# Kernel tuning notes

Measured on AMD Instinct MI355X. Metric: run time of the kernel, lower is better.

## Reference

```python
import jax, jax.numpy as jnp
import numpy as np

DIM = 512
H = 8
D = DIM // H  # head_dim = 64
B, N = 2, 2048


def setup_inputs() -> dict:
    key = jax.random.key(0)
    ks = jax.random.split(key, 12)
    s = 1.0 / np.sqrt(DIM)
    inp = {
        "x": jax.random.normal(ks[0], (B, N, DIM), jnp.float32),
        "geo_bias": jax.random.normal(ks[1], (B, H, N, N), jnp.float32),
        "Wq": jax.random.normal(ks[2], (DIM, DIM), jnp.float32) * s,
        "bq": jnp.zeros((DIM,), jnp.float32),
        "Wk": jax.random.normal(ks[3], (DIM, DIM), jnp.float32) * s,
        "bk": jnp.zeros((DIM,), jnp.float32),
        "Wv": jax.random.normal(ks[4], (DIM, DIM), jnp.float32) * s,
        "bv": jnp.zeros((DIM,), jnp.float32),
        "Wo": jax.random.normal(ks[5], (DIM, DIM), jnp.float32) * s,
        "bo": jnp.zeros((DIM,), jnp.float32),
    }
    return inp


def reference(x, geo_bias, Wq, bq, Wk, bk, Wv, bv, Wo, bo):
    # x: (B, N, dim); geo_bias: (B, H, N, N)
    scale = D ** -0.5
    q = (x @ Wq.T + bq).reshape(B, N, H, D)
    k = (x @ Wk.T + bk).reshape(B, N, H, D)
    v = (x @ Wv.T + bv).reshape(B, N, H, D)
    # scores: (B, H, N, N)
    attn = jnp.einsum("bihd,bjhd->bhij", q, k) * scale + geo_bias
    attn = jax.nn.softmax(attn, axis=-1)
    out = jnp.einsum("bhij,bjhd->bihd", attn, v).reshape(B, N, DIM)
    return out @ Wo.T + bo
```

## Files before the change

kernel.cpp:

```cpp
#include <hip/hip_runtime.h>
#include <math.h>

#define SCALE 0.125f

typedef __bf16 bf16;
typedef __bf16 bf16x8 __attribute__((ext_vector_type(8)));
typedef float f32x4 __attribute__((ext_vector_type(4)));

#define WS_XB   0u
#define WS_WB   4194304u
#define WS_Q    6291456u
#define WS_K    10485760u
#define WS_VT   14680064u
#define WS_AT   18874368u

__global__ __launch_bounds__(256) void convert_kernel(
    const float* __restrict__ x, const float* __restrict__ wq,
    const float* __restrict__ wk, const float* __restrict__ wv,
    const float* __restrict__ wo, bf16* __restrict__ xb, bf16* __restrict__ wb) {
  int i = blockIdx.x * 256 + threadIdx.x;
  const float4* src; bf16* dst; int off;
  if (i < 524288) { src = (const float4*)x; dst = xb; off = i; }
  else {
    int j = i - 524288;
    int wsel = j >> 16; off = j & 65535;
    const float* wl = wsel == 0 ? wq : wsel == 1 ? wk : wsel == 2 ? wv : wo;
    src = (const float4*)wl; dst = wb + (wsel << 18);
  }
  float4 v = src[off];
  union { bf16 h[4]; uint2 u; } tmp;
  tmp.h[0] = (bf16)v.x; tmp.h[1] = (bf16)v.y;
  tmp.h[2] = (bf16)v.z; tmp.h[3] = (bf16)v.w;
  ((uint2*)dst)[off] = tmp.u;
}

__global__ __launch_bounds__(256) void qkv_gemm(
    const bf16* __restrict__ xb, const bf16* __restrict__ wb,
    const float* __restrict__ bq, const float* __restrict__ bk,
    const float* __restrict__ bv, bf16* __restrict__ qws,
    bf16* __restrict__ kws, bf16* __restrict__ vtws) {
  __shared__ bf16 Al[128 * 40];
  __shared__ bf16 Bl[128 * 40];
  int t = threadIdx.x;
  int m0 = (blockIdx.x & 31) << 7;
  int n0 = (blockIdx.x >> 5) << 7;
  int lane = t & 63, w = t >> 6;
  int quad = lane >> 4, col = lane & 15;
  int mblk = (w >> 1) * 64, nblk = (w & 1) * 64;
  f32x4 acc[4][4] = {};
  for (int k0 = 0; k0 < 512; k0 += 32) {
    __syncthreads();
    for (int pass = 0; pass < 2; ++pass) {
      int c = t + (pass << 8);
      int row = c >> 2, part = c & 3;
      *(uint4*)&Al[row * 40 + part * 8] =
          *(const uint4*)&xb[(m0 + row) * 512 + k0 + part * 8];
      *(uint4*)&Bl[row * 40 + part * 8] =
          *(const uint4*)&wb[(n0 + row) * 512 + k0 + part * 8];
    }
    __syncthreads();
    bf16x8 af[4], bfv[4];
    for (int i = 0; i < 4; i++)
      af[i] = *(const bf16x8*)&Al[(mblk + i * 16 + col) * 40 + quad * 8];
    for (int i = 0; i < 4; i++)
      bfv[i] = *(const bf16x8*)&Bl[(nblk + i * 16 + col) * 40 + quad * 8];
    for (int mi = 0; mi < 4; mi++)
      for (int ni = 0; ni < 4; ni++)
        acc[mi][ni] = __builtin_amdgcn_mfma_f32_16x16x32_bf16(
            af[mi], bfv[ni], acc[mi][ni], 0, 0, 0);
  }
  for (int mi = 0; mi < 4; mi++)
    for (int ni = 0; ni < 4; ni++) {
      int n = n0 + nblk + ni * 16 + col;
      int wid = n >> 9, feat = n & 511;
      float bias = wid == 0 ? bq[feat] : wid == 1 ? bk[feat] : bv[feat];
      int h = feat >> 6, d = feat & 63;
      int mbase = m0 + mblk + mi * 16 + quad * 4;
      int bidx = mbase >> 11, seq0 = mbase & 2047;
      if (wid == 2) {
        union { bf16 h4[4]; ushort4 u4; } pk;
        for (int r = 0; r < 4; r++) pk.h4[r] = (bf16)(acc[mi][ni][r] + bias);
        *(ushort4*)&vtws[(size_t)((((bidx << 3) + h) << 6) + d) * 2048 + seq0] = pk.u4;
      } else {
        bf16* dst = wid == 0 ? qws : kws;
        for (int r = 0; r < 4; r++)
          dst[(size_t)((((bidx << 3) + h) << 11) + seq0 + r) * 64 + d] =
              (bf16)(acc[mi][ni][r] + bias);
      }
    }
}

__global__ __launch_bounds__(256, 2) void attn_kernel(
    const bf16* __restrict__ qws, const bf16* __restrict__ kws,
    const bf16* __restrict__ vtws, const float* __restrict__ gbias,
    bf16* __restrict__ attn) {
  __shared__ bf16 Kl[2][64 * 72];
  __shared__ bf16 Vl[2][64 * 72];
  __shared__ bf16 Pl[64 * 72];
  int t = threadIdx.x, lane = t & 63, w = t >> 6;
  int quad = lane >> 4, col = lane & 15;
  int bh = blockIdx.x >> 5, qt = blockIdx.x & 31;
  int q0 = qt << 6;
  const bf16* qbase = qws + (size_t)bh * 2048 * 64;
  const bf16* kbase = kws + (size_t)bh * 2048 * 64;
  const bf16* vbase = vtws + (size_t)bh * 64 * 2048;
  const float* bb = gbias + ((size_t)bh * 2048 + q0) * 2048;

  int srow = t >> 2;
  int scol = (t & 3) << 4;

  bf16x8 aq[2];
  for (int ks = 0; ks < 2; ++ks)
    aq[ks] = *(const bf16x8*)&qbase[(q0 + w * 16 + col) * 64 + ks * 32 + quad * 8];

  f32x4 o[4] = {};
  float mrow[4], lrow[4];
  for (int r = 0; r < 4; r++) { mrow[r] = -INFINITY; lrow[r] = 0.f; }

  float bc[2][16];
  for (int r = 0; r < 4; r++)
    for (int nt = 0; nt < 4; nt++) {
      const float* brow = bb + (size_t)(w * 16 + quad * 4 + r) * 2048;
      bc[0][r * 4 + nt] = brow[nt * 16 + col];
      bc[1][r * 4 + nt] = brow[64 + nt * 16 + col];
    }

  {
    *(uint4*)&Kl[0][srow * 72 + scol]     = *(const uint4*)&kbase[srow * 64 + scol];
    *(uint4*)&Kl[0][srow * 72 + scol + 8] = *(const uint4*)&kbase[srow * 64 + scol + 8];
    *(uint4*)&Vl[0][srow * 72 + scol]     = *(const uint4*)&vbase[srow * 2048 + scol];
    *(uint4*)&Vl[0][srow * 72 + scol + 8] = *(const uint4*)&vbase[srow * 2048 + scol + 8];
  }
  __syncthreads();

  for (int kt = 0; kt < 32; kt += 2) {
#pragma unroll
    for (int u = 0; u < 2; ++u) {
      const int cur = u;
      int kt_ = kt + u;
      int snxt = (kt_ + 1) << 6;

      uint4 kra = *(const uint4*)&kbase[(snxt + srow) * 64 + scol];
      uint4 krb = *(const uint4*)&kbase[(snxt + srow) * 64 + scol + 8];
      uint4 vra = *(const uint4*)&vbase[srow * 2048 + snxt + scol];
      uint4 vrb = *(const uint4*)&vbase[srow * 2048 + snxt + scol + 8];

      f32x4 s[4];
#pragma unroll
      for (int nt = 0; nt < 4; ++nt) {
        f32x4 a = {};
#pragma unroll
        for (int ks = 0; ks < 2; ++ks) {
          bf16x8 bk_ = *(const bf16x8*)&Kl[cur][(nt * 16 + col) * 72 + ks * 32 + quad * 8];
          a = __builtin_amdgcn_mfma_f32_16x16x32_bf16(aq[ks], bk_, a, 0, 0, 0);
        }
        s[nt] = a;
      }

      float p[4][4];
#pragma unroll
      for (int r = 0; r < 4; r++) {
        float sv[4];
        float mx = -INFINITY;
#pragma unroll
        for (int nt = 0; nt < 4; nt++) {
          sv[nt] = s[nt][r] * SCALE + bc[cur][r * 4 + nt];
          mx = fmaxf(mx, sv[nt]);
        }
#pragma unroll
        for (int d = 1; d < 16; d <<= 1) mx = fmaxf(mx, __shfl_xor(mx, d));
        float mnew = fmaxf(mrow[r], mx);
        float alpha = __expf(mrow[r] - mnew);
        float sum = 0.f;
#pragma unroll
        for (int nt = 0; nt < 4; nt++) {
          float e = __expf(sv[nt] - mnew);
          p[nt][r] = e; sum += e;
        }
#pragma unroll
        for (int d = 1; d < 16; d <<= 1) sum += __shfl_xor(sum, d);
        lrow[r] = lrow[r] * alpha + sum;
        mrow[r] = mnew;
#pragma unroll
        for (int dt = 0; dt < 4; ++dt) o[dt][r] *= alpha;
      }

      if (kt_ < 30) {
        int sb = (kt_ + 2) << 6;
#pragma unroll
        for (int r = 0; r < 4; r++) {
          const float* brow = bb + (size_t)(w * 16 + quad * 4 + r) * 2048 + sb;
#pragma unroll
          for (int nt = 0; nt < 4; nt++)
            bc[cur][r * 4 + nt] = brow[nt * 16 + col];
        }
      }

#pragma unroll
      for (int nt = 0; nt < 4; nt++)
#pragma unroll
        for (int r = 0; r < 4; r++)
          Pl[(w * 16 + quad * 4 + r) * 72 + nt * 16 + col] = (bf16)p[nt][r];

#pragma unroll
      for (int ks = 0; ks < 2; ++ks) {
        bf16x8 ap = *(const bf16x8*)&Pl[(w * 16 + col) * 72 + ks * 32 + quad * 8];
#pragma unroll
        for (int dt = 0; dt < 4; ++dt) {
          bf16x8 bv_ = *(const bf16x8*)&Vl[cur][(dt * 16 + col) * 72 + ks * 32 + quad * 8];
          o[dt] = __builtin_amdgcn_mfma_f32_16x16x32_bf16(ap, bv_, o[dt], 0, 0, 0);
        }
      }

      int nb = 1 - cur;
      *(uint4*)&Kl[nb][srow * 72 + scol]     = kra;
      *(uint4*)&Kl[nb][srow * 72 + scol + 8] = krb;
      *(uint4*)&Vl[nb][srow * 72 + scol]     = vra;
      *(uint4*)&Vl[nb][srow * 72 + scol + 8] = vrb;
      __syncthreads();
    }
  }

  bf16* obase = attn + (size_t)(bh >> 3) * 2048 * 512 + (bh & 7) * 64;
  for (int r = 0; r < 4; r++) {
    float inv = 1.f / lrow[r];
    int gq = q0 + w * 16 + quad * 4 + r;
    for (int dt = 0; dt < 4; ++dt)
      obase[(size_t)gq * 512 + dt * 16 + col] = (bf16)(o[dt][r] * inv);
  }
}

__global__ __launch_bounds__(256) void out_gemm(
    const bf16* __restrict__ ab, const bf16* __restrict__ wob,
    const float* __restrict__ bo, float* __restrict__ out) {
  __shared__ bf16 Al[128 * 40];
  __shared__ bf16 Bl[128 * 40];
  int t = threadIdx.x;
  int m0 = (blockIdx.x & 31) << 7;
  int n0 = (blockIdx.x >> 5) << 7;
  int lane = t & 63, w = t >> 6;
  int quad = lane >> 4, col = lane & 15;
  int mblk = (w >> 1) * 64, nblk = (w & 1) * 64;
  f32x4 acc[4][4] = {};
  for (int k0 = 0; k0 < 512; k0 += 32) {
    __syncthreads();
    for (int pass = 0; pass < 2; ++pass) {
      int c = t + (pass << 8);
      int row = c >> 2, part = c & 3;
      *(uint4*)&Al[row * 40 + part * 8] =
          *(const uint4*)&ab[(m0 + row) * 512 + k0 + part * 8];
      *(uint4*)&Bl[row * 40 + part * 8] =
          *(const uint4*)&wob[(n0 + row) * 512 + k0 + part * 8];
    }
    __syncthreads();
    bf16x8 af[4], bfv[4];
    for (int i = 0; i < 4; i++)
      af[i] = *(const bf16x8*)&Al[(mblk + i * 16 + col) * 40 + quad * 8];
    for (int i = 0; i < 4; i++)
      bfv[i] = *(const bf16x8*)&Bl[(nblk + i * 16 + col) * 40 + quad * 8];
    for (int mi = 0; mi < 4; mi++)
      for (int ni = 0; ni < 4; ni++)
        acc[mi][ni] = __builtin_amdgcn_mfma_f32_16x16x32_bf16(
            af[mi], bfv[ni], acc[mi][ni], 0, 0, 0);
  }
  for (int mi = 0; mi < 4; mi++)
    for (int ni = 0; ni < 4; ni++)
      for (int r = 0; r < 4; r++) {
        int m = m0 + mblk + mi * 16 + quad * 4 + r;
        int n = n0 + nblk + ni * 16 + col;
        out[(size_t)m * 512 + n] = acc[mi][ni][r] + bo[n];
      }
}

extern "C" void kernel_launch(void* const* d_in, const int* in_sizes, int n_in,
                              void* d_out, int out_size, void* d_ws, size_t ws_size,
                              hipStream_t stream) {
  const float* x  = (const float*)d_in[0];
  const float* gb = (const float*)d_in[1];
  const float* Wq = (const float*)d_in[2];
  const float* bq = (const float*)d_in[3];
  const float* Wk = (const float*)d_in[4];
  const float* bk = (const float*)d_in[5];
  const float* Wv = (const float*)d_in[6];
  const float* bv = (const float*)d_in[7];
  const float* Wo = (const float*)d_in[8];
  const float* bo = (const float*)d_in[9];
  float* out = (float*)d_out;
  char* ws = (char*)d_ws;
  bf16* xb   = (bf16*)(ws + WS_XB);
  bf16* wb   = (bf16*)(ws + WS_WB);
  bf16* qws  = (bf16*)(ws + WS_Q);
  bf16* kws  = (bf16*)(ws + WS_K);
  bf16* vtws = (bf16*)(ws + WS_VT);
  bf16* at   = (bf16*)(ws + WS_AT);

  hipLaunchKernelGGL(convert_kernel, dim3(3072), dim3(256), 0, stream,
                     x, Wq, Wk, Wv, Wo, xb, wb);
  hipLaunchKernelGGL(qkv_gemm, dim3(384), dim3(256), 0, stream,
                     xb, wb, bq, bk, bv, qws, kws, vtws);
  hipLaunchKernelGGL(attn_kernel, dim3(512), dim3(256), 0, stream,
                     qws, kws, vtws, gb, at);
  hipLaunchKernelGGL(out_gemm, dim3(128), dim3(256), 0, stream,
                     at, wb + 3 * 262144, bo, out);
}
```

Measured before the change: 443.4 us.

## Double-buffer GEMM tiles, stage geo bias through LDS, skip redundant softmax rescales

Both GEMMs switch to 128x64 tiles with register-prefetched, double-buffered LDS loads and twice as many blocks, so global loads overlap MFMA work and more CUs are busy. The attention kernel now loads the fp32 geo_bias tile with coalesced float4 reads into a swizzled LDS buffer, replacing strided per-lane scalar loads. It also skips the online-softmax rescale when no row max increases, and raises wave priority around the MFMA sections. The extra 32KB of LDS per block may reduce attention occupancy.

```diff
diff --git a/kernel.cpp b/kernel.cpp
--- a/kernel.cpp
+++ b/kernel.cpp
@@ -39,38 +39,50 @@
     const float* __restrict__ bq, const float* __restrict__ bk,
     const float* __restrict__ bv, bf16* __restrict__ qws,
     bf16* __restrict__ kws, bf16* __restrict__ vtws) {
-  __shared__ bf16 Al[128 * 40];
-  __shared__ bf16 Bl[128 * 40];
+  __shared__ bf16 Al[2][128 * 40];
+  __shared__ bf16 Bl[2][64 * 40];
   int t = threadIdx.x;
   int m0 = (blockIdx.x & 31) << 7;
-  int n0 = (blockIdx.x >> 5) << 7;
+  int n0 = (blockIdx.x >> 5) << 6;
   int lane = t & 63, w = t >> 6;
   int quad = lane >> 4, col = lane & 15;
-  int mblk = (w >> 1) * 64, nblk = (w & 1) * 64;
-  f32x4 acc[4][4] = {};
-  for (int k0 = 0; k0 < 512; k0 += 32) {
+  int mblk = (w >> 1) * 64, nblk = (w & 1) * 32;
+  int arow = t >> 1, apart = (t & 1) << 1;
+  int brow = t >> 2, bpart = t & 3;
+  const bf16* ag = &xb[(m0 + arow) * 512 + apart * 8];
+  const bf16* bg = &wb[(n0 + brow) * 512 + bpart * 8];
+  f32x4 acc[4][2] = {};
+  uint4 ra0 = *(const uint4*)ag;
+  uint4 ra1 = *(const uint4*)(ag + 8);
+  uint4 rb  = *(const uint4*)bg;
+  for (int it = 0; it < 16; ++it) {
+    int cur = it & 1;
+    *(uint4*)&Al[cur][arow * 40 + apart * 8]     = ra0;
+    *(uint4*)&Al[cur][arow * 40 + apart * 8 + 8] = ra1;
+    *(uint4*)&Bl[cur][brow * 40 + bpart * 8]     = rb;
+    if (it < 15) {
+      int k0 = (it + 1) << 5;
+      ra0 = *(const uint4*)(ag + k0);
+      ra1 = *(const uint4*)(ag + k0 + 8);
+      rb  = *(const uint4*)(bg + k0);
+    }
     __syncthreads();
-    for (int pass = 0; pass < 2; ++pass) {
-      int c = t + (pass << 8);
-      int row = c >> 2, part = c & 3;
-      *(uint4*)&Al[row * 40 + part * 8] =
-          *(const uint4*)&xb[(m0 + row) * 512 + k0 + part * 8];
-      *(uint4*)&Bl[row * 40 + part * 8] =
-          *(const uint4*)&wb[(n0 + row) * 512 + k0 + part * 8];
-    }
-    __syncthreads();
-    bf16x8 af[4], bfv[4];
+    bf16x8 af[4], bfv[2];
+#pragma unroll
     for (int i = 0; i < 4; i++)
-      af[i] = *(const bf16x8*)&Al[(mblk + i * 16 + col) * 40 + quad * 8];
-    for (int i = 0; i < 4; i++)
-      bfv[i] = *(const bf16x8*)&Bl[(nblk + i * 16 + col) * 40 + quad * 8];
+      af[i] = *(const bf16x8*)&Al[cur][(mblk + i * 16 + col) * 40 + quad * 8];
+#pragma unroll
+    for (int i = 0; i < 2; i++)
+      bfv[i] = *(const bf16x8*)&Bl[cur][(nblk + i * 16 + col) * 40 + quad * 8];
+#pragma unroll
     for (int mi = 0; mi < 4; mi++)
-      for (int ni = 0; ni < 4; ni++)
+#pragma unroll
+      for (int ni = 0; ni < 2; ni++)
         acc[mi][ni] = __builtin_amdgcn_mfma_f32_16x16x32_bf16(
             af[mi], bfv[ni], acc[mi][ni], 0, 0, 0);
   }
   for (int mi = 0; mi < 4; mi++)
-    for (int ni = 0; ni < 4; ni++) {
+    for (int ni = 0; ni < 2; ni++) {
       int n = n0 + nblk + ni * 16 + col;
       int wid = n >> 9, feat = n & 511;
       float bias = wid == 0 ? bq[feat] : wid == 1 ? bk[feat] : bv[feat];
@@ -97,6 +109,7 @@
   __shared__ bf16 Kl[2][64 * 72];
   __shared__ bf16 Vl[2][64 * 72];
   __shared__ bf16 Pl[64 * 72];
+  __shared__ float Bb[2][64 * 64];
   int t = threadIdx.x, lane = t & 63, w = t >> 6;
   int quad = lane >> 4, col = lane & 15;
   int bh = blockIdx.x >> 5, qt = blockIdx.x & 31;
@@ -106,119 +119,124 @@
   const bf16* vbase = vtws + (size_t)bh * 64 * 2048;
   const float* bb = gbias + ((size_t)bh * 2048 + q0) * 2048;
 
-  int srow = t >> 2;
-  int scol = (t & 3) << 4;
+  int srow = t >> 2, scol = (t & 3) << 4;
+  int brow0 = t >> 4, bcol4 = t & 15;
 
   bf16x8 aq[2];
+#pragma unroll
   for (int ks = 0; ks < 2; ++ks)
     aq[ks] = *(const bf16x8*)&qbase[(q0 + w * 16 + col) * 64 + ks * 32 + quad * 8];
 
   f32x4 o[4] = {};
   float mrow[4], lrow[4];
+#pragma unroll
   for (int r = 0; r < 4; r++) { mrow[r] = -INFINITY; lrow[r] = 0.f; }
 
-  float bc[2][16];
-  for (int r = 0; r < 4; r++)
-    for (int nt = 0; nt < 4; nt++) {
-      const float* brow = bb + (size_t)(w * 16 + quad * 4 + r) * 2048;
-      bc[0][r * 4 + nt] = brow[nt * 16 + col];
-      bc[1][r * 4 + nt] = brow[64 + nt * 16 + col];
-    }
-
-  {
-    *(uint4*)&Kl[0][srow * 72 + scol]     = *(const uint4*)&kbase[srow * 64 + scol];
-    *(uint4*)&Kl[0][srow * 72 + scol + 8] = *(const uint4*)&kbase[srow * 64 + scol + 8];
-    *(uint4*)&Vl[0][srow * 72 + scol]     = *(const uint4*)&vbase[srow * 2048 + scol];
-    *(uint4*)&Vl[0][srow * 72 + scol + 8] = *(const uint4*)&vbase[srow * 2048 + scol + 8];
+  *(uint4*)&Kl[0][srow * 72 + scol]     = *(const uint4*)&kbase[srow * 64 + scol];
+  *(uint4*)&Kl[0][srow * 72 + scol + 8] = *(const uint4*)&kbase[srow * 64 + scol + 8];
+  *(uint4*)&Vl[0][srow * 72 + scol]     = *(const uint4*)&vbase[srow * 2048 + scol];
+  *(uint4*)&Vl[0][srow * 72 + scol + 8] = *(const uint4*)&vbase[srow * 2048 + scol + 8];
+#pragma unroll
+  for (int p = 0; p < 4; ++p) {
+    int row = brow0 + (p << 4);
+    int sw = (row >> 2) & 3;
+    *(float4*)&Bb[0][row * 64 + ((bcol4 ^ (sw << 2)) << 2)] =
+        *(const float4*)&bb[(size_t)row * 2048 + (bcol4 << 2)];
   }
   __syncthreads();
 
-  for (int kt = 0; kt < 32; kt += 2) {
-#pragma unroll
-    for (int u = 0; u < 2; ++u) {
-      const int cur = u;
-      int kt_ = kt + u;
-      int snxt = (kt_ + 1) << 6;
-
-      uint4 kra = *(const uint4*)&kbase[(snxt + srow) * 64 + scol];
-      uint4 krb = *(const uint4*)&kbase[(snxt + srow) * 64 + scol + 8];
-      uint4 vra = *(const uint4*)&vbase[srow * 2048 + snxt + scol];
-      uint4 vrb = *(const uint4*)&vbase[srow * 2048 + snxt + scol + 8];
-
-      f32x4 s[4];
-#pragma unroll
-      for (int nt = 0; nt < 4; ++nt) {
-        f32x4 a = {};
-#pragma unroll
-        for (int ks = 0; ks < 2; ++ks) {
-          bf16x8 bk_ = *(const bf16x8*)&Kl[cur][(nt * 16 + col) * 72 + ks * 32 + quad * 8];
-          a = __builtin_amdgcn_mfma_f32_16x16x32_bf16(aq[ks], bk_, a, 0, 0, 0);
-        }
-        s[nt] = a;
-      }
-
-      float p[4][4];
-#pragma unroll
-      for (int r = 0; r < 4; r++) {
-        float sv[4];
-        float mx = -INFINITY;
-#pragma unroll
-        for (int nt = 0; nt < 4; nt++) {
-          sv[nt] = s[nt][r] * SCALE + bc[cur][r * 4 + nt];
-          mx = fmaxf(mx, sv[nt]);
-        }
-#pragma unroll
-        for (int d = 1; d < 16; d <<= 1) mx = fmaxf(mx, __shfl_xor(mx, d));
+  uint4 kra, krb, vra, vrb;
+  float4 br4[4];
+  for (int kt = 0; kt < 32; ++kt) {
+    int cur = kt & 1, nb = cur ^ 1;
+    bool pre = kt < 31;
+    if (pre) {
+      int snxt = (kt + 1) << 6;
+      kra = *(const uint4*)&kbase[(snxt + srow) * 64 + scol];
+      krb = *(const uint4*)&kbase[(snxt + srow) * 64 + scol + 8];
+      vra = *(const uint4*)&vbase[srow * 2048 + snxt + scol];
+      vrb = *(const uint4*)&vbase[srow * 2048 + snxt + scol + 8];
+#pragma unroll
+      for (int p = 0; p < 4; ++p)
+        br4[p] = *(const float4*)&bb[(size_t)(brow0 + (p << 4)) * 2048 + snxt + (bcol4 << 2)];
+    }
+
+    f32x4 s[4];
+    __builtin_amdgcn_s_setprio(1);
+#pragma unroll
+    for (int nt = 0; nt < 4; ++nt) {
+      f32x4 a = {};
+#pragma unroll
+      for (int ks = 0; ks < 2; ++ks) {
+        bf16x8 bk_ = *(const bf16x8*)&Kl[cur][(nt * 16 + col) * 72 + ks * 32 + quad * 8];
+        a = __builtin_amdgcn_mfma_f32_16x16x32_bf16(aq[ks], bk_, a, 0, 0, 0);
+      }
+      s[nt] = a;
+    }
+    __builtin_amdgcn_s_setprio(0);
+
+    int rbase = (w * 16 + quad * 4) * 64;
+#pragma unroll
+    for (int r = 0; r < 4; r++) {
+      float sv[4];
+#pragma unroll
+      for (int nt = 0; nt < 4; nt++)
+        sv[nt] = s[nt][r] * SCALE +
+                 Bb[cur][rbase + r * 64 + ((nt ^ quad) << 4) + col];
+      float mx = fmaxf(fmaxf(sv[0], sv[1]), fmaxf(sv[2], sv[3]));
+#pragma unroll
+      for (int d = 1; d < 16; d <<= 1) mx = fmaxf(mx, __shfl_xor(mx, d));
+      if (!__all(mx <= mrow[r])) {
         float mnew = fmaxf(mrow[r], mx);
         float alpha = __expf(mrow[r] - mnew);
-        float sum = 0.f;
-#pragma unroll
-        for (int nt = 0; nt < 4; nt++) {
-          float e = __expf(sv[nt] - mnew);
-          p[nt][r] = e; sum += e;
-        }
-#pragma unroll
-        for (int d = 1; d < 16; d <<= 1) sum += __shfl_xor(sum, d);
-        lrow[r] = lrow[r] * alpha + sum;
         mrow[r] = mnew;
+        lrow[r] *= alpha;
 #pragma unroll
         for (int dt = 0; dt < 4; ++dt) o[dt][r] *= alpha;
       }
-
-      if (kt_ < 30) {
-        int sb = (kt_ + 2) << 6;
-#pragma unroll
-        for (int r = 0; r < 4; r++) {
-          const float* brow = bb + (size_t)(w * 16 + quad * 4 + r) * 2048 + sb;
-#pragma unroll
-          for (int nt = 0; nt < 4; nt++)
-            bc[cur][r * 4 + nt] = brow[nt * 16 + col];
-        }
-      }
-
-#pragma unroll
-      for (int nt = 0; nt < 4; nt++)
-#pragma unroll
-        for (int r = 0; r < 4; r++)
-          Pl[(w * 16 + quad * 4 + r) * 72 + nt * 16 + col] = (bf16)p[nt][r];
-
-#pragma unroll
-      for (int ks = 0; ks < 2; ++ks) {
-        bf16x8 ap = *(const bf16x8*)&Pl[(w * 16 + col) * 72 + ks * 32 + quad * 8];
-#pragma unroll
-        for (int dt = 0; dt < 4; ++dt) {
-          bf16x8 bv_ = *(const bf16x8*)&Vl[cur][(dt * 16 + col) * 72 + ks * 32 + quad * 8];
-          o[dt] = __builtin_amdgcn_mfma_f32_16x16x32_bf16(ap, bv_, o[dt], 0, 0, 0);
-        }
-      }
-
-      int nb = 1 - cur;
+      float sum = 0.f;
+#pragma unroll
+      for (int nt = 0; nt < 4; nt++) {
+        float e = __expf(sv[nt] - mrow[r]);
+        s[nt][r] = e;
+        sum += e;
+      }
+#pragma unroll
+      for (int d = 1; d < 16; d <<= 1) sum += __shfl_xor(sum, d);
+      lrow[r] += sum;
+    }
+
+#pragma unroll
+    for (int nt = 0; nt < 4; nt++)
+#pragma unroll
+      for (int r = 0; r < 4; r++)
+        Pl[(w * 16 + quad * 4 + r) * 72 + nt * 16 + col] = (bf16)s[nt][r];
+
+    __builtin_amdgcn_s_setprio(1);
+#pragma unroll
+    for (int ks = 0; ks < 2; ++ks) {
+      bf16x8 ap = *(const bf16x8*)&Pl[(w * 16 + col) * 72 + ks * 32 + quad * 8];
+#pragma unroll
+      for (int dt = 0; dt < 4; ++dt) {
+        bf16x8 bv_ = *(const bf16x8*)&Vl[cur][(dt * 16 + col) * 72 + ks * 32 + quad * 8];
+        o[dt] = __builtin_amdgcn_mfma_f32_16x16x32_bf16(ap, bv_, o[dt], 0, 0, 0);
+      }
+    }
+    __builtin_amdgcn_s_setprio(0);
+
+    if (pre) {
       *(uint4*)&Kl[nb][srow * 72 + scol]     = kra;
       *(uint4*)&Kl[nb][srow * 72 + scol + 8] = krb;
       *(uint4*)&Vl[nb][srow * 72 + scol]     = vra;
       *(uint4*)&Vl[nb][srow * 72 + scol + 8] = vrb;
-      __syncthreads();
-    }
+#pragma unroll
+      for (int p = 0; p < 4; ++p) {
+        int row = brow0 + (p << 4);
+        int sw = (row >> 2) & 3;
+        *(float4*)&Bb[nb][row * 64 + ((bcol4 ^ (sw << 2)) << 2)] = br4[p];
+      }
+    }
+    __syncthreads();
   }
 
   bf16* obase = attn + (size_t)(bh >> 3) * 2048 * 512 + (bh & 7) * 64;
@@ -233,38 +251,50 @@
 __global__ __launch_bounds__(256) void out_gemm(
     const bf16* __restrict__ ab, const bf16* __restrict__ wob,
     const float* __restrict__ bo, float* __restrict__ out) {
-  __shared__ bf16 Al[128 * 40];
-  __shared__ bf16 Bl[128 * 40];
+  __shared__ bf16 Al[2][128 * 40];
+  __shared__ bf16 Bl[2][64 * 40];
   int t = threadIdx.x;
   int m0 = (blockIdx.x & 31) << 7;
-  int n0 = (blockIdx.x >> 5) << 7;
+  int n0 = (blockIdx.x >> 5) << 6;
   int lane = t & 63, w = t >> 6;
   int quad = lane >> 4, col = lane & 15;
-  int mblk = (w >> 1) * 64, nblk = (w & 1) * 64;
-  f32x4 acc[4][4] = {};
-  for (int k0 = 0; k0 < 512; k0 += 32) {
+  int mblk = (w >> 1) * 64, nblk = (w & 1) * 32;
+  int arow = t >> 1, apart = (t & 1) << 1;
+  int brow = t >> 2, bpart = t & 3;
+  const bf16* ag = &ab[(m0 + arow) * 512 + apart * 8];
+  const bf16* bg = &wob[(n0 + brow) * 512 + bpart * 8];
+  f32x4 acc[4][2] = {};
+  uint4 ra0 = *(const uint4*)ag;
+  uint4 ra1 = *(const uint4*)(ag + 8);
+  uint4 rb  = *(const uint4*)bg;
+  for (int it = 0; it < 16; ++it) {
+    int cur = it & 1;
+    *(uint4*)&Al[cur][arow * 40 + apart * 8]     = ra0;
+    *(uint4*)&Al[cur][arow * 40 + apart * 8 + 8] = ra1;
+    *(uint4*)&Bl[cur][brow * 40 + bpart * 8]     = rb;
+    if (it < 15) {
+      int k0 = (it + 1) << 5;
+      ra0 = *(const uint4*)(ag + k0);
+      ra1 = *(const uint4*)(ag + k0 + 8);
+      rb  = *(const uint4*)(bg + k0);
+    }
     __syncthreads();
-    for (int pass = 0; pass < 2; ++pass) {
-      int c = t + (pass << 8);
-      int row = c >> 2, part = c & 3;
-      *(uint4*)&Al[row * 40 + part * 8] =
-          *(const uint4*)&ab[(m0 + row) * 512 + k0 + part * 8];
-      *(uint4*)&Bl[row * 40 + part * 8] =
-          *(const uint4*)&wob[(n0 + row) * 512 + k0 + part * 8];
-    }
-    __syncthreads();
-    bf16x8 af[4], bfv[4];
+    bf16x8 af[4], bfv[2];
+#pragma unroll
     for (int i = 0; i < 4; i++)
-      af[i] = *(const bf16x8*)&Al[(mblk + i * 16 + col) * 40 + quad * 8];
-    for (int i = 0; i < 4; i++)
-      bfv[i] = *(const bf16x8*)&Bl[(nblk + i * 16 + col) * 40 + quad * 8];
+      af[i] = *(const bf16x8*)&Al[cur][(mblk + i * 16 + col) * 40 + quad * 8];
+#pragma unroll
+    for (int i = 0; i < 2; i++)
+      bfv[i] = *(const bf16x8*)&Bl[cur][(nblk + i * 16 + col) * 40 + quad * 8];
+#pragma unroll
     for (int mi = 0; mi < 4; mi++)
-      for (int ni = 0; ni < 4; ni++)
+#pragma unroll
+      for (int ni = 0; ni < 2; ni++)
         acc[mi][ni] = __builtin_amdgcn_mfma_f32_16x16x32_bf16(
             af[mi], bfv[ni], acc[mi][ni], 0, 0, 0);
   }
   for (int mi = 0; mi < 4; mi++)
-    for (int ni = 0; ni < 4; ni++)
+    for (int ni = 0; ni < 2; ni++)
       for (int r = 0; r < 4; r++) {
         int m = m0 + mblk + mi * 16 + quad * 4 + r;
         int n = n0 + nblk + ni * 16 + col;
@@ -296,10 +326,10 @@
 
   hipLaunchKernelGGL(convert_kernel, dim3(3072), dim3(256), 0, stream,
                      x, Wq, Wk, Wv, Wo, xb, wb);
-  hipLaunchKernelGGL(qkv_gemm, dim3(384), dim3(256), 0, stream,
+  hipLaunchKernelGGL(qkv_gemm, dim3(768), dim3(256), 0, stream,
                      xb, wb, bq, bk, bv, qws, kws, vtws);
   hipLaunchKernelGGL(attn_kernel, dim3(512), dim3(256), 0, stream,
                      qws, kws, vtws, gb, at);
-  hipLaunchKernelGGL(out_gemm, dim3(128), dim3(256), 0, stream,
+  hipLaunchKernelGGL(out_gemm, dim3(256), dim3(256), 0, stream,
                      at, wb + 3 * 262144, bo, out);
 }
```

Measured after the change: 429.6 us. 3.1% less time.
